# Performance work log

Hardware: AMD Instinct MI355X
Metric: run time of the kernel (lower is better)

## Reference

```python
import jax, jax.numpy as jnp
import numpy as np

N_SIGMA = 2
N_CLASS = 8
FG_WEIGHT = jnp.array([10., 10., 10., 40., 80., 100., 60., 20.], dtype=jnp.float32)
W_INST, W_VAR, W_SEED = 1.0, 10.0, 1.0
MIN_PIXELS = 128


def lovasz_hinge_flat(logits, labels):
    # logits, labels: [P] flat; labels in {0,1}
    signs = 2.0 * labels - 1.0
    errors = 1.0 - logits * signs
    order = jnp.argsort(-errors)  # descending
    errors_sorted = errors[order]
    gt_sorted = labels[order]
    gts = gt_sorted.sum()
    inter = gts - jnp.cumsum(gt_sorted)
    union = gts + jnp.cumsum(1.0 - gt_sorted)
    jac = 1.0 - inter / union
    grad = jnp.concatenate([jac[:1], jac[1:] - jac[:-1]])
    return jnp.dot(jax.nn.relu(errors_sorted), jax.lax.stop_gradient(grad))


def setup_inputs() -> dict:
    key = jax.random.key(0)
    k1, k2, k3, k4 = jax.random.split(key, 4)
    B, H, W, N = 2, 512, 1024, 8
    prediction = jax.random.normal(k1, (B, 12, H, W), dtype=jnp.float32)
    bbox = jax.random.randint(k2, (B, 9, H, W), 0, 2, dtype=jnp.int32)
    masks = jax.random.randint(k3, (B, N, H, W), 0, 2, dtype=jnp.int32)
    cls_ids = jax.random.randint(k4, (B, N), 0, 8, dtype=jnp.int32)
    return {"prediction": prediction, "bbox": bbox, "masks": masks, "cls_ids": cls_ids}


def _forward(prediction, bbox, masks, cls_ids):
    B, C, H, W = prediction.shape
    N = masks.shape[1]
    sg = jax.lax.stop_gradient
    # coordinate map: full 2048/1024 linspace sliced to [:W]/[:H], as in the buffer
    xm = jnp.linspace(0.0, 2.0, 2048, dtype=prediction.dtype)[:W]
    ym = jnp.linspace(0.0, 1.0, 1024, dtype=prediction.dtype)[:H]
    xym = jnp.stack([jnp.broadcast_to(xm[None, :], (H, W)),
                     jnp.broadcast_to(ym[:, None], (H, W))], axis=0)  # [2,H,W]

    spatial_emb = jnp.tanh(prediction[:, 0:2]) + xym[None]            # [B,2,H,W]
    sigma = prediction[:, 2:2 + N_SIGMA]                               # [B,2,H,W]
    seed = jax.nn.sigmoid(prediction[:, 2 + N_SIGMA:2 + N_SIGMA + N_CLASS])  # [B,8,H,W]

    # background seed loss: sum over cls 1..8 of seed[cls-1]^2 where bbox[cls]==0
    bg = bbox[:, 1:9] == 0                                             # [B,8,H,W]
    seed_bg = jnp.sum(jnp.where(bg, seed * seed, 0.0), axis=(1, 2, 3))  # [B]

    m = (masks > 0).astype(prediction.dtype)                           # [B,N,H,W]
    cnt = m.sum(axis=(2, 3))                                           # [B,N]
    valid = (cnt >= MIN_PIXELS).astype(prediction.dtype)               # [B,N]
    cnt_safe = jnp.maximum(cnt, 1.0)

    # per-instance masked means (to_center=False -> center from spatial_emb)
    center = jnp.einsum('bnhw,bchw->bnc', m, spatial_emb) / cnt_safe[..., None]  # [B,N,2]
    s_mean = jnp.einsum('bnhw,bchw->bnc', m, sigma) / cnt_safe[..., None]        # [B,N,2]

    # var loss: mean over [n_sigma, P] of (sigma_in - s.detach())^2
    diff2 = (sigma[:, None] - sg(s_mean)[..., None, None]) ** 2        # [B,N,2,H,W]
    var_inst = jnp.einsum('bnchw,bnhw->bn', diff2, m) / (N_SIGMA * cnt_safe)

    s_exp = jnp.exp(s_mean * 10.0)                                     # [B,N,2]
    d2 = (spatial_emb[:, None] - center[..., None, None]) ** 2         # [B,N,2,H,W]
    dist = jnp.exp(-jnp.einsum('bnchw,bnc->bnhw', d2, s_exp))          # [B,N,H,W]

    # lovasz hinge per instance on dist*2-1 vs mask
    logits = (dist * 2.0 - 1.0).reshape(B * N, H * W)
    labels = m.reshape(B * N, H * W)
    lov = jax.vmap(lovasz_hinge_flat)(logits, labels).reshape(B, N)    # [B,N]

    # foreground seed loss
    seed_cls = jnp.take_along_axis(seed, cls_ids[..., None, None].astype(jnp.int32), axis=1)  # [B,N,H,W]
    fw = FG_WEIGHT[cls_ids]                                            # [B,N]
    seed_fg = fw * jnp.einsum('bnhw,bnhw->bn', m, (seed_cls - sg(dist)) ** 2)

    obj = valid.sum(axis=1)                                            # [B]
    obj_safe = jnp.maximum(obj, 1.0)
    inst_l = jnp.sum(lov * valid, axis=1) / obj_safe
    var_l = jnp.sum(var_inst * valid, axis=1) / obj_safe
    seed_l = (seed_bg + jnp.sum(seed_fg * valid, axis=1)) / (H * W)
    loss = jnp.mean(W_INST * inst_l + W_VAR * var_l + W_SEED * seed_l)
    return loss


def reference(prediction, bbox, masks, cls_ids):
    return _forward(prediction, bbox, masks, cls_ids)
```

## Files before the change

kernel.cpp:

```cpp
#include <hip/hip_runtime.h>
#include <cstdint>
#include <cstddef>

#define HW 524288
#define HW4 131072
#define NBIN 2048


__device__ __forceinline__ float wred(float v) {
#pragma unroll
  for (int o = 32; o > 0; o >>= 1) v += __shfl_xor(v, o, 64);
  return v;
}

__device__ __forceinline__ float fsig(float x) {
  return __builtin_amdgcn_rcpf(1.f + expf(-x));
}

__global__ __launch_bounds__(256) void pass1(
    const float* __restrict__ pred, const int* __restrict__ masks,
    double* __restrict__ acc)
{
  const int b = blockIdx.y;
  const int tid = threadIdx.x;
  const int g = blockIdx.x * 256 + tid;
  const float4* pb4 = (const float4*)(pred + (size_t)b * 12 * HW);
  const int4*   mk4 = (const int4*)(masks + (size_t)b * 8 * HW);

  int idx = g << 2;
  int h = idx >> 10, w = idx & 1023;
  float4 p0 = pb4[g];
  float4 p1 = pb4[HW4 + g];
  float4 s0 = pb4[2 * HW4 + g];
  float4 s1 = pb4[3 * HW4 + g];
  int4 mv[8];
#pragma unroll
  for (int n = 0; n < 8; n++) mv[n] = mk4[n * HW4 + g];

  float p0v[4] = {p0.x, p0.y, p0.z, p0.w}, p1v[4] = {p1.x, p1.y, p1.z, p1.w};
  float s0v[4] = {s0.x, s0.y, s0.z, s0.w}, s1v[4] = {s1.x, s1.y, s1.z, s1.w};
  float exv[4], eyv[4];
#pragma unroll
  for (int j = 0; j < 4; j++) {
    exv[j] = tanhf(p0v[j]) + (float)((w + j) * (2.0 / 2047.0));
    eyv[j] = tanhf(p1v[j]) + (float)(h * (1.0 / 1023.0));
  }

  float c[8] = {0}, cx[8] = {0}, cy[8] = {0}, sx[8] = {0}, sy[8] = {0},
        sxx[8] = {0}, syy[8] = {0};
#pragma unroll
  for (int n = 0; n < 8; n++) {
    int mvv[4] = {mv[n].x, mv[n].y, mv[n].z, mv[n].w};
#pragma unroll
    for (int j = 0; j < 4; j++) {
      float mf = (mvv[j] > 0) ? 1.f : 0.f;
      c[n] += mf; cx[n] += mf * exv[j]; cy[n] += mf * eyv[j];
      sx[n] += mf * s0v[j]; sy[n] += mf * s1v[j];
      sxx[n] += mf * s0v[j] * s0v[j]; syy[n] += mf * s1v[j] * s1v[j];
    }
  }

  __shared__ float red[4][56];
  int lane = tid & 63, wid = tid >> 6;
#pragma unroll
  for (int n = 0; n < 8; n++) {
    float r0 = wred(c[n]),  r1 = wred(cx[n]), r2 = wred(cy[n]),
          r3 = wred(sx[n]), r4 = wred(sy[n]), r5 = wred(sxx[n]),
          r6 = wred(syy[n]);
    if (lane == 0) {
      red[wid][n * 7 + 0] = r0; red[wid][n * 7 + 1] = r1;
      red[wid][n * 7 + 2] = r2; red[wid][n * 7 + 3] = r3;
      red[wid][n * 7 + 4] = r4; red[wid][n * 7 + 5] = r5;
      red[wid][n * 7 + 6] = r6;
    }
  }
  __syncthreads();
  if (tid < 56) {
    float s = red[0][tid] + red[1][tid] + red[2][tid] + red[3][tid];
    int n = tid / 7, q = tid % 7;
    atomicAdd(&acc[((size_t)b * 8 + n) * 8 + q], (double)s);
  }
}

__global__ __launch_bounds__(1024) void pass3(
    const float* __restrict__ pred, const int* __restrict__ bbox,
    const int* __restrict__ masks, const int* __restrict__ cls_ids,
    double* __restrict__ acc, double* __restrict__ seedbg,
    unsigned* __restrict__ ghist)
{
  const int seg = blockIdx.y;
  const int b = seg >> 3, n = seg & 7;
  const int tid = threadIdx.x;
  __shared__ unsigned hist[NBIN * 2];
  __shared__ float redf[16][2];
  for (int j = tid; j < NBIN * 2; j += 1024) hist[j] = 0;

  const double* a = acc + seg * 8;
  double cntd = a[0];
  double cs = cntd < 1.0 ? 1.0 : cntd;
  float cxv = (float)(a[1] / cs), cyv = (float)(a[2] / cs);
  float sex = expf((float)(a[3] / cs) * 10.f);
  float sey = expf((float)(a[4] / cs) * 10.f);
  int cls = cls_ids[b * 8 + n];
  const float4* pb4 = (const float4*)(pred + (size_t)b * 12 * HW);
  const float4* sp4 = pb4 + (size_t)(4 + cls) * HW4;
  const float4* sb4 = pb4 + (size_t)(4 + n) * HW4;
  const int4*   mp4 = (const int4*)(masks + (size_t)seg * HW);
  const int4*   bb4 = (const int4*)(bbox + (size_t)b * 9 * HW) + (1 + n) * HW4;
  __syncthreads();

  float sf = 0.f, sbg = 0.f;
  int gbase = blockIdx.x * 4096;
#pragma unroll
  for (int i = 0; i < 4; i++) {
    int g = gbase + i * 1024 + tid;
    int idx = g << 2;
    int h = idx >> 10, w = idx & 1023;
    float4 p0 = pb4[g];
    float4 p1 = pb4[HW4 + g];
    int4 mv = mp4[g];
    float4 sv = sp4[g];
    float4 sb = sb4[g];
    int4 bv = bb4[g];
    float p0v[4] = {p0.x, p0.y, p0.z, p0.w}, p1v[4] = {p1.x, p1.y, p1.z, p1.w};
    float svv[4] = {sv.x, sv.y, sv.z, sv.w}, sbv[4] = {sb.x, sb.y, sb.z, sb.w};
    int mvv[4] = {mv.x, mv.y, mv.z, mv.w}, bvv[4] = {bv.x, bv.y, bv.z, bv.w};
#pragma unroll
    for (int j = 0; j < 4; j++) {
      int m = (mvv[j] > 0) ? 1 : 0;
      float ex = tanhf(p0v[j]) + (float)((w + j) * (2.0 / 2047.0));
      float ey = tanhf(p1v[j]) + (float)(h * (1.0 / 1023.0));
      float dx = ex - cxv, dy = ey - cyv;
      float d = expf(-(dx * dx * sex + dy * dy * sey));
      float sg = fsig(svv[j]);
      float df = sg - d;
      sf += m ? df * df : 0.f;
      float sgb = fsig(sbv[j]);
      sbg += (bvv[j] == 0) ? sgb * sgb : 0.f;
      float e = m ? 2.f - 2.f * d : 2.f * d;
      int k = (int)(e * 1024.f); k = k > (NBIN - 1) ? (NBIN - 1) : k;
      atomicAdd(&hist[k * 2 + m], 1u);
    }
  }
  __syncthreads();

  unsigned* gh = ghist + (size_t)seg * NBIN * 2;
  for (int j = tid; j < NBIN * 2; j += 1024) {
    unsigned v = hist[j];
    if (v) atomicAdd(&gh[j], v);
  }

  float r0 = wred(sf), r1 = wred(sbg);
  int lane = tid & 63, wid = tid >> 6;
  if (lane == 0) { redf[wid][0] = r0; redf[wid][1] = r1; }
  __syncthreads();
  if (tid == 0) {
    float t = 0.f;
    for (int w2 = 0; w2 < 16; w2++) t += redf[w2][0];
    atomicAdd(&acc[seg * 8 + 7], (double)t);
  } else if (tid == 64) {
    float t = 0.f;
    for (int w2 = 0; w2 < 16; w2++) t += redf[w2][1];
    atomicAdd(&seedbg[b], (double)t);
  }
}

__global__ __launch_bounds__(256) void pass4(
    const unsigned* __restrict__ ghist, const double* __restrict__ acc,
    const double* __restrict__ seedbg, const int* __restrict__ cls_ids,
    float* __restrict__ lov, unsigned* __restrict__ ctr,
    float* __restrict__ out)
{
  const int seg = blockIdx.x;
  const int tid = threadIdx.x;
  const int lane = tid & 63, wid = tid >> 6;
  __shared__ __align__(16) unsigned lh[NBIN * 2];
  __shared__ unsigned wc[4], wp[4];
  __shared__ double sred[4];

  const uint4* gh4 = (const uint4*)(ghist + (size_t)seg * NBIN * 2);
#pragma unroll
  for (int i = 0; i < 4; i++)
    ((uint4*)lh)[i * 256 + tid] = gh4[i * 256 + tid];
  __syncthreads();

  double G = acc[seg * 8 + 0];

  unsigned cntT = 0, posT = 0;
#pragma unroll
  for (int i = 0; i < 8; i++) {
    int kk = (NBIN - 1) - tid * 8 - i;
    unsigned h0 = lh[2 * kk], h1 = lh[2 * kk + 1];
    cntT += h0 + h1; posT += h1;
  }
  unsigned ic = cntT, ip = posT;
  for (int o = 1; o < 64; o <<= 1) {
    unsigned yc = __shfl_up(ic, o, 64), yp = __shfl_up(ip, o, 64);
    if (lane >= o) { ic += yc; ip += yp; }
  }
  if (lane == 63) { wc[wid] = ic; wp[wid] = ip; }
  __syncthreads();
  unsigned oc = 0, op = 0;
  for (int w2 = 0; w2 < wid; w2++) { oc += wc[w2]; op += wp[w2]; }
  unsigned p = oc + ic - cntT, C = op + ip - posT;

  double S = 0.0;
#pragma unroll
  for (int i = 0; i < 8; i++) {
    int kk = (NBIN - 1) - tid * 8 - i;
    unsigned n1 = lh[2 * kk + 1], n0 = lh[2 * kk];
    double ec = (kk + 0.5) * (1.0 / 1024.0);
    if (n1) {
      S += (double)n1 * ec / (G + (double)(p - C));
      p += n1; C += n1;
    }
    if (n0) {
      double rem = G - (double)C;
      if (rem > 0.0) {
        double aa = G + (double)(p - C);
        S += ec * rem * (1.0 / aa - 1.0 / (aa + (double)n0));
      }
      p += n0;
    }
  }
#pragma unroll
  for (int o = 32; o > 0; o >>= 1) S += __shfl_xor(S, o, 64);
  if (lane == 0) sred[wid] = S;
  __syncthreads();

  if (tid == 0) {
    double St = sred[0] + sred[1] + sred[2] + sred[3];
    atomicExch(&lov[seg], (float)St);
    __threadfence();
    unsigned old = atomicAdd(ctr, 1u);
    if (old == 15u) {
      __threadfence();
      const float FG[8] = {10.f, 10.f, 10.f, 40.f, 80.f, 100.f, 60.f, 20.f};
      double total = 0.0;
      for (int b = 0; b < 2; b++) {
        double obj = 0, inst = 0, varl = 0, sfg = 0;
        for (int n = 0; n < 8; n++) {
          int s = b * 8 + n;
          const double* a = acc + s * 8;
          double cnt = a[0];
          double cs = cnt < 1.0 ? 1.0 : cnt;
          double smx = a[3] / cs, smy = a[4] / cs;
          double var = ((a[5] - cnt * smx * smx) + (a[6] - cnt * smy * smy)) /
                       (2.0 * cs);
          double v = (cnt >= 128.0) ? 1.0 : 0.0;
          double lv = (double)atomicAdd(&lov[s], 0.0f);
          obj += v;
          inst += lv * v;
          varl += var * v;
          sfg += (double)FG[cls_ids[s]] * a[7] * v;
        }
        double objs = obj < 1.0 ? 1.0 : obj;
        double seedl = (seedbg[b] + sfg) / (double)HW;
        total += inst / objs + 10.0 * (varl / objs) + seedl;
      }
      out[0] = (float)(0.5 * total);
    }
  }
}

extern "C" void kernel_launch(void* const* d_in, const int* in_sizes, int n_in,
                              void* d_out, int out_size, void* d_ws, size_t ws_size,
                              hipStream_t stream)
{
  (void)in_sizes; (void)n_in; (void)out_size; (void)ws_size;
  const float* pred  = (const float*)d_in[0];
  const int*   bbox  = (const int*)d_in[1];
  const int*   masks = (const int*)d_in[2];
  const int*   cls   = (const int*)d_in[3];

  char* ws = (char*)d_ws;
  double*   acc    = (double*)(ws + 0);
  double*   seedbg = (double*)(ws + 1024);
  float*    lov    = (float*)(ws + 1040);
  unsigned* ctr    = (unsigned*)(ws + 1104);
  unsigned* ghist  = (unsigned*)(ws + 4096);

  hipMemsetAsync(d_ws, 0, 266240, stream);
  pass1<<<dim3(512, 2), 256, 0, stream>>>(pred, masks, acc);
  pass3<<<dim3(32, 16), 1024, 0, stream>>>(pred, bbox, masks, cls, acc, seedbg, ghist);
  pass4<<<16, 256, 0, stream>>>(ghist, acc, seedbg, cls, lov, ctr, (float*)d_out);
}
```

Measured before the change: 186.7 us.

## Process all instances per pixel block in pass3 with packed halved histograms

Pass3 now has each block cover one pixel tile across all 8 instances of a batch item, so pred channels 0-1 and the tanh embedding are loaded and computed once per pixel instead of once per instance. Each seed channel is also read once for the background term. The Lovasz histogram shrinks to 1024 bins, with positive and negative counts packed into one 32-bit shared word and flushed as 64-bit global atomics, which reduces atomic traffic and memset size. Fast exp/tanh intrinsics replace the libm calls, and pass1 handles two tiles per thread. The risks are coarser histogram resolution, which affects Lovasz accuracy, and the 16-bit packed counts, which could overflow if a block puts more than 65535 pixels of one class into a bin.

```diff
diff --git a/kernel.cpp b/kernel.cpp
--- a/kernel.cpp
+++ b/kernel.cpp
@@ -4,7 +4,7 @@
 
 #define HW 524288
 #define HW4 131072
-#define NBIN 2048
+#define NBIN 1024
 
 
 __device__ __forceinline__ float wred(float v) {
@@ -14,7 +14,10 @@
 }
 
 __device__ __forceinline__ float fsig(float x) {
-  return __builtin_amdgcn_rcpf(1.f + expf(-x));
+  return __builtin_amdgcn_rcpf(1.f + __expf(-x));
+}
+__device__ __forceinline__ float ftanh(float x) {
+  return 1.f - 2.f * __builtin_amdgcn_rcpf(__expf(2.f * x) + 1.f);
 }
 
 __global__ __launch_bounds__(256) void pass1(
@@ -23,40 +26,43 @@
 {
   const int b = blockIdx.y;
   const int tid = threadIdx.x;
-  const int g = blockIdx.x * 256 + tid;
   const float4* pb4 = (const float4*)(pred + (size_t)b * 12 * HW);
   const int4*   mk4 = (const int4*)(masks + (size_t)b * 8 * HW);
 
-  int idx = g << 2;
-  int h = idx >> 10, w = idx & 1023;
-  float4 p0 = pb4[g];
-  float4 p1 = pb4[HW4 + g];
-  float4 s0 = pb4[2 * HW4 + g];
-  float4 s1 = pb4[3 * HW4 + g];
-  int4 mv[8];
-#pragma unroll
-  for (int n = 0; n < 8; n++) mv[n] = mk4[n * HW4 + g];
-
-  float p0v[4] = {p0.x, p0.y, p0.z, p0.w}, p1v[4] = {p1.x, p1.y, p1.z, p1.w};
-  float s0v[4] = {s0.x, s0.y, s0.z, s0.w}, s1v[4] = {s1.x, s1.y, s1.z, s1.w};
-  float exv[4], eyv[4];
-#pragma unroll
-  for (int j = 0; j < 4; j++) {
-    exv[j] = tanhf(p0v[j]) + (float)((w + j) * (2.0 / 2047.0));
-    eyv[j] = tanhf(p1v[j]) + (float)(h * (1.0 / 1023.0));
-  }
-
   float c[8] = {0}, cx[8] = {0}, cy[8] = {0}, sx[8] = {0}, sy[8] = {0},
         sxx[8] = {0}, syy[8] = {0};
-#pragma unroll
-  for (int n = 0; n < 8; n++) {
-    int mvv[4] = {mv[n].x, mv[n].y, mv[n].z, mv[n].w};
+
+#pragma unroll
+  for (int k = 0; k < 2; k++) {
+    const int g = blockIdx.x * 512 + k * 256 + tid;
+    int idx = g << 2;
+    int h = idx >> 10, w = idx & 1023;
+    float4 p0 = pb4[g];
+    float4 p1 = pb4[HW4 + g];
+    float4 s0 = pb4[2 * HW4 + g];
+    float4 s1 = pb4[3 * HW4 + g];
+    int4 mv[8];
+#pragma unroll
+    for (int n = 0; n < 8; n++) mv[n] = mk4[n * HW4 + g];
+
+    float p0v[4] = {p0.x, p0.y, p0.z, p0.w}, p1v[4] = {p1.x, p1.y, p1.z, p1.w};
+    float s0v[4] = {s0.x, s0.y, s0.z, s0.w}, s1v[4] = {s1.x, s1.y, s1.z, s1.w};
+    float exv[4], eyv[4];
 #pragma unroll
     for (int j = 0; j < 4; j++) {
-      float mf = (mvv[j] > 0) ? 1.f : 0.f;
-      c[n] += mf; cx[n] += mf * exv[j]; cy[n] += mf * eyv[j];
-      sx[n] += mf * s0v[j]; sy[n] += mf * s1v[j];
-      sxx[n] += mf * s0v[j] * s0v[j]; syy[n] += mf * s1v[j] * s1v[j];
+      exv[j] = ftanh(p0v[j]) + (float)((w + j) * (2.0 / 2047.0));
+      eyv[j] = ftanh(p1v[j]) + (float)(h * (1.0 / 1023.0));
+    }
+#pragma unroll
+    for (int n = 0; n < 8; n++) {
+      int mvv[4] = {mv[n].x, mv[n].y, mv[n].z, mv[n].w};
+#pragma unroll
+      for (int j = 0; j < 4; j++) {
+        float mf = (mvv[j] > 0) ? 1.f : 0.f;
+        c[n] += mf; cx[n] += mf * exv[j]; cy[n] += mf * eyv[j];
+        sx[n] += mf * s0v[j]; sy[n] += mf * s1v[j];
+        sxx[n] += mf * s0v[j] * s0v[j]; syy[n] += mf * s1v[j] * s1v[j];
+      }
     }
   }
 
@@ -86,87 +92,107 @@
     const float* __restrict__ pred, const int* __restrict__ bbox,
     const int* __restrict__ masks, const int* __restrict__ cls_ids,
     double* __restrict__ acc, double* __restrict__ seedbg,
-    unsigned* __restrict__ ghist)
+    unsigned long long* __restrict__ ghist)
 {
-  const int seg = blockIdx.y;
-  const int b = seg >> 3, n = seg & 7;
+  const int b = blockIdx.y;
   const int tid = threadIdx.x;
-  __shared__ unsigned hist[NBIN * 2];
-  __shared__ float redf[16][2];
-  for (int j = tid; j < NBIN * 2; j += 1024) hist[j] = 0;
-
-  const double* a = acc + seg * 8;
-  double cntd = a[0];
-  double cs = cntd < 1.0 ? 1.0 : cntd;
-  float cxv = (float)(a[1] / cs), cyv = (float)(a[2] / cs);
-  float sex = expf((float)(a[3] / cs) * 10.f);
-  float sey = expf((float)(a[4] / cs) * 10.f);
-  int cls = cls_ids[b * 8 + n];
+  __shared__ unsigned hist[8 * NBIN];
+  __shared__ float cxs[8], cys[8], sxs[8], sys[8];
+  __shared__ int clss[8];
+  __shared__ float redf[16][9];
+  for (int j = tid; j < 8 * NBIN; j += 1024) hist[j] = 0;
+  if (tid < 8) {
+    const double* a = acc + ((size_t)b * 8 + tid) * 8;
+    double cs = a[0] < 1.0 ? 1.0 : a[0];
+    cxs[tid] = (float)(a[1] / cs);
+    cys[tid] = (float)(a[2] / cs);
+    sxs[tid] = __expf((float)(a[3] / cs) * 10.f);
+    sys[tid] = __expf((float)(a[4] / cs) * 10.f);
+    clss[tid] = cls_ids[b * 8 + tid];
+  }
+  __syncthreads();
+
   const float4* pb4 = (const float4*)(pred + (size_t)b * 12 * HW);
-  const float4* sp4 = pb4 + (size_t)(4 + cls) * HW4;
-  const float4* sb4 = pb4 + (size_t)(4 + n) * HW4;
-  const int4*   mp4 = (const int4*)(masks + (size_t)seg * HW);
-  const int4*   bb4 = (const int4*)(bbox + (size_t)b * 9 * HW) + (1 + n) * HW4;
-  __syncthreads();
-
-  float sf = 0.f, sbg = 0.f;
-  int gbase = blockIdx.x * 4096;
-#pragma unroll
-  for (int i = 0; i < 4; i++) {
-    int g = gbase + i * 1024 + tid;
-    int idx = g << 2;
-    int h = idx >> 10, w = idx & 1023;
-    float4 p0 = pb4[g];
-    float4 p1 = pb4[HW4 + g];
-    int4 mv = mp4[g];
-    float4 sv = sp4[g];
-    float4 sb = sb4[g];
-    int4 bv = bb4[g];
-    float p0v[4] = {p0.x, p0.y, p0.z, p0.w}, p1v[4] = {p1.x, p1.y, p1.z, p1.w};
-    float svv[4] = {sv.x, sv.y, sv.z, sv.w}, sbv[4] = {sb.x, sb.y, sb.z, sb.w};
-    int mvv[4] = {mv.x, mv.y, mv.z, mv.w}, bvv[4] = {bv.x, bv.y, bv.z, bv.w};
+  const int4*   mk4 = (const int4*)(masks + (size_t)b * 8 * HW);
+  const int4*   bb4 = (const int4*)(bbox + (size_t)b * 9 * HW + HW);
+  const int g = blockIdx.x * 1024 + tid;
+  int idx = g << 2;
+  int h = idx >> 10, w = idx & 1023;
+
+  float4 p0 = pb4[g];
+  float4 p1 = pb4[HW4 + g];
+  float p0v[4] = {p0.x, p0.y, p0.z, p0.w}, p1v[4] = {p1.x, p1.y, p1.z, p1.w};
+  float ex[4], ey[4];
+#pragma unroll
+  for (int j = 0; j < 4; j++) {
+    ex[j] = ftanh(p0v[j]) + (float)((w + j) * (2.0 / 2047.0));
+    ey[j] = ftanh(p1v[j]) + (float)(h * (1.0 / 1023.0));
+  }
+
+  float sbg = 0.f;
+#pragma unroll
+  for (int cc = 0; cc < 8; cc++) {
+    float4 sv = pb4[(4 + cc) * HW4 + g];
+    int4 bv = bb4[cc * HW4 + g];
+    float svv[4] = {sv.x, sv.y, sv.z, sv.w};
+    int bvv[4] = {bv.x, bv.y, bv.z, bv.w};
+#pragma unroll
+    for (int j = 0; j < 4; j++) {
+      float s = fsig(svv[j]);
+      sbg += (bvv[j] == 0) ? s * s : 0.f;
+    }
+  }
+
+  float sf[8];
+#pragma unroll
+  for (int n = 0; n < 8; n++) sf[n] = 0.f;
+#pragma unroll
+  for (int n = 0; n < 8; n++) {
+    int4 mv = mk4[n * HW4 + g];
+    float4 sv = pb4[(4 + clss[n]) * HW4 + g];
+    float cxn = cxs[n], cyn = cys[n], sxn = sxs[n], syn = sys[n];
+    int mvv[4] = {mv.x, mv.y, mv.z, mv.w};
+    float svv[4] = {sv.x, sv.y, sv.z, sv.w};
 #pragma unroll
     for (int j = 0; j < 4; j++) {
       int m = (mvv[j] > 0) ? 1 : 0;
-      float ex = tanhf(p0v[j]) + (float)((w + j) * (2.0 / 2047.0));
-      float ey = tanhf(p1v[j]) + (float)(h * (1.0 / 1023.0));
-      float dx = ex - cxv, dy = ey - cyv;
-      float d = expf(-(dx * dx * sex + dy * dy * sey));
-      float sg = fsig(svv[j]);
-      float df = sg - d;
-      sf += m ? df * df : 0.f;
-      float sgb = fsig(sbv[j]);
-      sbg += (bvv[j] == 0) ? sgb * sgb : 0.f;
+      float dx = ex[j] - cxn, dy = ey[j] - cyn;
+      float d = __expf(-(dx * dx * sxn + dy * dy * syn));
+      float df = fsig(svv[j]) - d;
+      sf[n] += m ? df * df : 0.f;
       float e = m ? 2.f - 2.f * d : 2.f * d;
-      int k = (int)(e * 1024.f); k = k > (NBIN - 1) ? (NBIN - 1) : k;
-      atomicAdd(&hist[k * 2 + m], 1u);
-    }
-  }
-  __syncthreads();
-
-  unsigned* gh = ghist + (size_t)seg * NBIN * 2;
-  for (int j = tid; j < NBIN * 2; j += 1024) {
+      int k = (int)(e * 512.f); k = k > (NBIN - 1) ? (NBIN - 1) : k;
+      atomicAdd(&hist[n * NBIN + k], m ? 65536u : 1u);
+    }
+  }
+  __syncthreads();
+
+  unsigned long long* gh = ghist + (size_t)b * 8 * NBIN;
+  for (int j = tid; j < 8 * NBIN; j += 1024) {
     unsigned v = hist[j];
-    if (v) atomicAdd(&gh[j], v);
-  }
-
-  float r0 = wred(sf), r1 = wred(sbg);
+    if (v)
+      atomicAdd(&gh[j], (unsigned long long)(v & 0xffffu) |
+                        ((unsigned long long)(v >> 16) << 32));
+  }
+
   int lane = tid & 63, wid = tid >> 6;
-  if (lane == 0) { redf[wid][0] = r0; redf[wid][1] = r1; }
-  __syncthreads();
-  if (tid == 0) {
+#pragma unroll
+  for (int n = 0; n < 8; n++) {
+    float r = wred(sf[n]);
+    if (lane == 0) redf[wid][n] = r;
+  }
+  { float r = wred(sbg); if (lane == 0) redf[wid][8] = r; }
+  __syncthreads();
+  if (tid < 9) {
     float t = 0.f;
-    for (int w2 = 0; w2 < 16; w2++) t += redf[w2][0];
-    atomicAdd(&acc[seg * 8 + 7], (double)t);
-  } else if (tid == 64) {
-    float t = 0.f;
-    for (int w2 = 0; w2 < 16; w2++) t += redf[w2][1];
-    atomicAdd(&seedbg[b], (double)t);
+    for (int w2 = 0; w2 < 16; w2++) t += redf[w2][tid];
+    if (tid < 8) atomicAdd(&acc[((size_t)b * 8 + tid) * 8 + 7], (double)t);
+    else atomicAdd(&seedbg[b], (double)t);
   }
 }
 
 __global__ __launch_bounds__(256) void pass4(
-    const unsigned* __restrict__ ghist, const double* __restrict__ acc,
+    const unsigned long long* __restrict__ ghist, const double* __restrict__ acc,
     const double* __restrict__ seedbg, const int* __restrict__ cls_ids,
     float* __restrict__ lov, unsigned* __restrict__ ctr,
     float* __restrict__ out)
@@ -178,9 +204,9 @@
   __shared__ unsigned wc[4], wp[4];
   __shared__ double sred[4];
 
-  const uint4* gh4 = (const uint4*)(ghist + (size_t)seg * NBIN * 2);
-#pragma unroll
-  for (int i = 0; i < 4; i++)
+  const uint4* gh4 = (const uint4*)(ghist + (size_t)seg * NBIN);
+#pragma unroll
+  for (int i = 0; i < 2; i++)
     ((uint4*)lh)[i * 256 + tid] = gh4[i * 256 + tid];
   __syncthreads();
 
@@ -188,8 +214,8 @@
 
   unsigned cntT = 0, posT = 0;
 #pragma unroll
-  for (int i = 0; i < 8; i++) {
-    int kk = (NBIN - 1) - tid * 8 - i;
+  for (int i = 0; i < 4; i++) {
+    int kk = (NBIN - 1) - tid * 4 - i;
     unsigned h0 = lh[2 * kk], h1 = lh[2 * kk + 1];
     cntT += h0 + h1; posT += h1;
   }
@@ -206,10 +232,10 @@
 
   double S = 0.0;
 #pragma unroll
-  for (int i = 0; i < 8; i++) {
-    int kk = (NBIN - 1) - tid * 8 - i;
+  for (int i = 0; i < 4; i++) {
+    int kk = (NBIN - 1) - tid * 4 - i;
     unsigned n1 = lh[2 * kk + 1], n0 = lh[2 * kk];
-    double ec = (kk + 0.5) * (1.0 / 1024.0);
+    double ec = (kk + 0.5) * (1.0 / 512.0);
     if (n1) {
       S += (double)n1 * ec / (G + (double)(p - C));
       p += n1; C += n1;
@@ -274,14 +300,14 @@
   const int*   cls   = (const int*)d_in[3];
 
   char* ws = (char*)d_ws;
-  double*   acc    = (double*)(ws + 0);
-  double*   seedbg = (double*)(ws + 1024);
-  float*    lov    = (float*)(ws + 1040);
-  unsigned* ctr    = (unsigned*)(ws + 1104);
-  unsigned* ghist  = (unsigned*)(ws + 4096);
-
-  hipMemsetAsync(d_ws, 0, 266240, stream);
-  pass1<<<dim3(512, 2), 256, 0, stream>>>(pred, masks, acc);
-  pass3<<<dim3(32, 16), 1024, 0, stream>>>(pred, bbox, masks, cls, acc, seedbg, ghist);
+  double*             acc    = (double*)(ws + 0);
+  double*             seedbg = (double*)(ws + 1024);
+  float*              lov    = (float*)(ws + 1040);
+  unsigned*           ctr    = (unsigned*)(ws + 1104);
+  unsigned long long* ghist  = (unsigned long long*)(ws + 4096);
+
+  hipMemsetAsync(d_ws, 0, 135168, stream);
+  pass1<<<dim3(256, 2), 256, 0, stream>>>(pred, masks, acc);
+  pass3<<<dim3(128, 2), 1024, 0, stream>>>(pred, bbox, masks, cls, acc, seedbg, ghist);
   pass4<<<16, 256, 0, stream>>>(ghist, acc, seedbg, cls, lov, ctr, (float*)d_out);
 }
```

Measured after the change: 192.7 us. +3.2%, slower.
